# Performance work log

Measured on AMD Instinct MI355X. Metric: run time of the kernel, lower is better.

Reference implementation:

```python
import jax, jax.numpy as jnp
import numpy as np

N, E = 100000, 1600000
IN, HID, EMB = 128, 256, 64


def setup_inputs() -> dict:
    key = jax.random.key(0)
    ks = jax.random.split(key, 8)
    x = jax.random.normal(ks[0], (N, IN), dtype=jnp.float32)
    edge_index = jax.random.randint(ks[1], (2, E), 0, N, dtype=jnp.int64)
    def glorot(k, fan_in, fan_out):
        lim = np.sqrt(6.0 / (fan_in + fan_out)).astype(np.float32)
        return jax.random.uniform(k, (fan_in, fan_out), jnp.float32, -lim, lim)
    return {
        "x": x,
        "edge_index": edge_index,
        "W1": glorot(ks[2], IN, HID), "b1": jnp.zeros((HID,), jnp.float32),
        "W2": glorot(ks[3], HID, HID), "b2": jnp.zeros((HID,), jnp.float32),
        "W3": glorot(ks[4], HID, EMB), "b3": jnp.zeros((EMB,), jnp.float32),
    }


def reference(x, edge_index, W1, b1, W2, b2, W3, b3):
    n = x.shape[0]
    # add self loops (PyG GCNConv default, fill_value=1)
    loops = jnp.arange(n, dtype=edge_index.dtype)
    src = jnp.concatenate([edge_index[0], loops])
    dst = jnp.concatenate([edge_index[1], loops])
    # symmetric normalization D^-1/2 A_hat D^-1/2 (degree at target)
    deg = jax.ops.segment_sum(jnp.ones_like(src, dtype=x.dtype), dst, num_segments=n)
    dinv = jnp.where(deg > 0, deg ** -0.5, 0.0)
    norm = (dinv[src] * dinv[dst])[:, None]  # [E+N, 1]

    def conv(h, W, b):
        h = h @ W                               # [N, out]
        agg = jax.ops.segment_sum(h[src] * norm, dst, num_segments=n)
        return agg + b

    h = jax.nn.relu(conv(x, W1, b1))   # dropout: identity in eval mode
    h = jax.nn.relu(conv(h, W2, b2))
    h = conv(h, W3, b3)
    # L2-normalize rows (F.normalize, eps=1e-12)
    nrm = jnp.linalg.norm(h, axis=1, keepdims=True)
    return h / jnp.maximum(nrm, 1e-12)
```

## Files before the change

### kernel.cpp

```cpp
#include <hip/hip_runtime.h>
#include <cstddef>
#include <cstdint>

constexpr int IN_F  = 128;
constexpr int HID_F = 256;
constexpr int EMB_F = 64;

typedef float  f32x4  __attribute__((ext_vector_type(4)));
typedef short  bf16x8 __attribute__((ext_vector_type(8)));
typedef unsigned short ushort_t;
typedef ushort_t u16x4 __attribute__((ext_vector_type(4)));
typedef ushort_t u16x2 __attribute__((ext_vector_type(2)));

__device__ inline float bf2f(ushort_t u) {
  union { unsigned i; float f; } c; c.i = ((unsigned)u) << 16; return c.f;
}
__device__ inline ushort_t f2bf(float f) {
  union { float f; unsigned i; } c; c.f = f;
  unsigned r = c.i + 0x7FFFu + ((c.i >> 16) & 1u);
  return (ushort_t)(r >> 16);
}


__global__ void k_setup(const float* __restrict__ W1, const float* __restrict__ W2,
                        const float* __restrict__ W3,
                        ushort_t* __restrict__ W1t, ushort_t* __restrict__ W2t,
                        ushort_t* __restrict__ W3t) {
  constexpr int c1 = IN_F * HID_F;
  constexpr int c2 = c1 + HID_F * HID_F;
  constexpr int c3 = c2 + HID_F * EMB_F;
  int i = blockIdx.x * blockDim.x + threadIdx.x;
  if (i < c1) {
    int k = i / HID_F, nn = i - k * HID_F;
    W1t[(size_t)nn * IN_F + k] = f2bf(W1[i]);
  } else if (i < c2) {
    int j = i - c1;
    int k = j / HID_F, nn = j - k * HID_F;
    W2t[(size_t)nn * HID_F + k] = f2bf(W2[j]);
  } else if (i < c3) {
    int j = i - c2;
    int k = j / EMB_F, nn = j - k * EMB_F;
    W3t[(size_t)nn * HID_F + k] = f2bf(W3[j]);
  }
}


constexpr int NBKT = 512;
constexpr int CHUNK = 16384;

__global__ __launch_bounds__(512) void k_hist(const int* __restrict__ dst,
                                              int* __restrict__ ghist, int e) {
  __shared__ int cnt[NBKT];
  cnt[threadIdx.x] = 0;
  __syncthreads();
  int i0 = blockIdx.x * CHUNK;
  int i1 = min(e, i0 + CHUNK);
  for (int i = i0 + threadIdx.x; i < i1; i += 512)
    atomicAdd(&cnt[dst[i] >> 8], 1);
  __syncthreads();
  int c = cnt[threadIdx.x];
  if (c > 0) atomicAdd(&ghist[threadIdx.x], c);
}

__global__ __launch_bounds__(512) void k_bscan(const int* __restrict__ ghist,
                                               int* __restrict__ bstart,
                                               int* __restrict__ gcursor) {
  __shared__ int s[NBKT];
  int v = ghist[threadIdx.x];
  s[threadIdx.x] = v;
  __syncthreads();
#pragma unroll
  for (int off = 1; off < NBKT; off <<= 1) {
    int t = (threadIdx.x >= off) ? s[threadIdx.x - off] : 0;
    __syncthreads();
    s[threadIdx.x] += t;
    __syncthreads();
  }
  int ex = s[threadIdx.x] - v;
  bstart[threadIdx.x] = ex;
  gcursor[threadIdx.x] = ex;
}

__global__ __launch_bounds__(512) void k_passA(const int* __restrict__ src,
                                               const int* __restrict__ dst,
                                               int* __restrict__ gcursor,
                                               unsigned* __restrict__ staged, int e) {
  __shared__ int cnt[NBKT];
  __shared__ int base[NBKT];
  cnt[threadIdx.x] = 0;
  __syncthreads();
  int i0 = blockIdx.x * CHUNK;
  int i1 = min(e, i0 + CHUNK);
  for (int i = i0 + threadIdx.x; i < i1; i += 512)
    atomicAdd(&cnt[dst[i] >> 8], 1);
  __syncthreads();
  int c = cnt[threadIdx.x];
  base[threadIdx.x] = (c > 0) ? atomicAdd(&gcursor[threadIdx.x], c) : 0;
  cnt[threadIdx.x] = 0;
  __syncthreads();
  for (int i = i0 + threadIdx.x; i < i1; i += 512) {
    int d = dst[i];
    int b = d >> 8;
    int lp = atomicAdd(&cnt[b], 1);
    staged[base[b] + lp] = ((unsigned)(d & 255) << 17) | (unsigned)src[i];
  }
}

__global__ __launch_bounds__(256) void k_B1(const unsigned* __restrict__ staged,
                                            const int* __restrict__ bstart,
                                            const int* __restrict__ ghist,
                                            int* __restrict__ edgedeg,
                                            float* __restrict__ dinv, int n) {
  __shared__ int cnt[256];
  cnt[threadIdx.x] = 0;
  __syncthreads();
  int b = blockIdx.x;
  int beg = bstart[b], end = beg + ghist[b];
  for (int i = beg + threadIdx.x; i < end; i += 256)
    atomicAdd(&cnt[staged[i] >> 17], 1);
  __syncthreads();
  int node = (b << 8) + threadIdx.x;
  if (node < n) {
    int c = cnt[threadIdx.x];
    edgedeg[node] = c;
    dinv[node] = rsqrtf((float)(c + 1));
  }
}

__global__ __launch_bounds__(256) void k_B2(const unsigned* __restrict__ staged,
                                            const int* __restrict__ bstart,
                                            const int* __restrict__ ghist,
                                            const int* __restrict__ rowptr,
                                            int* __restrict__ csr, int n) {
  __shared__ int cur[256];
  cur[threadIdx.x] = 0;
  __syncthreads();
  int b = blockIdx.x;
  int beg = bstart[b], end = beg + ghist[b];
  int nb0 = b << 8;
  for (int i = beg + threadIdx.x; i < end; i += 256) {
    unsigned p = staged[i];
    int l = (int)(p >> 17);
    int s = (int)(p & 0x1FFFFu);
    int pos = rowptr[nb0 + l] + atomicAdd(&cur[l], 1);
    csr[pos] = s;
  }
}


__global__ void k_scan1(const int* __restrict__ edgedeg, int* __restrict__ rowptr,
                        int* __restrict__ bsum, int n) {
  __shared__ int s[256];
  int i = blockIdx.x * 256 + threadIdx.x;
  int v = (i < n) ? edgedeg[i] : 0;
  s[threadIdx.x] = v;
  __syncthreads();
#pragma unroll
  for (int off = 1; off < 256; off <<= 1) {
    int t = (threadIdx.x >= off) ? s[threadIdx.x - off] : 0;
    __syncthreads();
    s[threadIdx.x] += t;
    __syncthreads();
  }
  if (i < n) rowptr[i] = s[threadIdx.x] - v;
  if (threadIdx.x == 255) bsum[blockIdx.x] = s[255];
}

__global__ void k_scan2(int* __restrict__ bsum, int nb) {
  __shared__ int s[512];
  int v = (threadIdx.x < nb) ? bsum[threadIdx.x] : 0;
  s[threadIdx.x] = v;
  __syncthreads();
#pragma unroll
  for (int off = 1; off < 512; off <<= 1) {
    int t = (threadIdx.x >= off) ? s[threadIdx.x - off] : 0;
    __syncthreads();
    s[threadIdx.x] += t;
    __syncthreads();
  }
  if (threadIdx.x < nb) bsum[threadIdx.x] = s[threadIdx.x] - v;
}

__global__ void k_scan3(int* __restrict__ rowptr, const int* __restrict__ bsum,
                        int n, int e) {
  int i = blockIdx.x * blockDim.x + threadIdx.x;
  if (i < n) rowptr[i] += bsum[i >> 8];
  else if (i == n) rowptr[n] = e;
}


__global__ void k_xconv(const float* __restrict__ x, const float* __restrict__ dinv,
                        ushort_t* __restrict__ xb, int n4 ) {
  int i = blockIdx.x * blockDim.x + threadIdx.x;
  if (i >= n4) return;
  float s = dinv[i >> 5];
  float4 v = reinterpret_cast<const float4*>(x)[i];
  u16x4 o;
  o[0] = f2bf(v.x * s); o[1] = f2bf(v.y * s); o[2] = f2bf(v.z * s); o[3] = f2bf(v.w * s);
  reinterpret_cast<u16x4*>(xb)[i] = o;
}


__global__ __launch_bounds__(256) void k_gather1(
    const ushort_t* __restrict__ t, ushort_t* __restrict__ outp,
    const int* __restrict__ rowptr, const int* __restrict__ csr, int n) {
  int wid = (blockIdx.x * blockDim.x + threadIdx.x) >> 6;
  int lane = threadIdx.x & 63;
  if (wid >= n) return;
  float a0, a1;
  {
    u16x2 v = *reinterpret_cast<const u16x2*>(t + (size_t)wid * IN_F + lane * 2);
    a0 = bf2f(v[0]); a1 = bf2f(v[1]);
  }
  int beg = rowptr[wid], end = rowptr[wid + 1];
  int j = beg;
  for (; j + 3 < end; j += 4) {
    int s0 = csr[j], s1 = csr[j + 1], s2 = csr[j + 2], s3 = csr[j + 3];
    u16x2 v0 = *reinterpret_cast<const u16x2*>(t + (size_t)s0 * IN_F + lane * 2);
    u16x2 v1 = *reinterpret_cast<const u16x2*>(t + (size_t)s1 * IN_F + lane * 2);
    u16x2 v2 = *reinterpret_cast<const u16x2*>(t + (size_t)s2 * IN_F + lane * 2);
    u16x2 v3 = *reinterpret_cast<const u16x2*>(t + (size_t)s3 * IN_F + lane * 2);
    a0 += bf2f(v0[0]); a1 += bf2f(v0[1]);
    a0 += bf2f(v1[0]); a1 += bf2f(v1[1]);
    a0 += bf2f(v2[0]); a1 += bf2f(v2[1]);
    a0 += bf2f(v3[0]); a1 += bf2f(v3[1]);
  }
  for (; j < end; ++j) {
    int s0 = csr[j];
    u16x2 v0 = *reinterpret_cast<const u16x2*>(t + (size_t)s0 * IN_F + lane * 2);
    a0 += bf2f(v0[0]); a1 += bf2f(v0[1]);
  }
  u16x2 o; o[0] = f2bf(a0); o[1] = f2bf(a1);
  *reinterpret_cast<u16x2*>(outp + (size_t)wid * IN_F + lane * 2) = o;
}

__global__ __launch_bounds__(256) void k_gather2(
    const ushort_t* __restrict__ t, ushort_t* __restrict__ outp,
    const int* __restrict__ rowptr, const int* __restrict__ csr,
    const float* __restrict__ dinv, const float* __restrict__ bias, int n) {
  int wid = (blockIdx.x * blockDim.x + threadIdx.x) >> 6;
  int lane = threadIdx.x & 63;
  if (wid >= n) return;
  float acc[4];
  {
    u16x4 v = *reinterpret_cast<const u16x4*>(t + (size_t)wid * HID_F + lane * 4);
#pragma unroll
    for (int k = 0; k < 4; ++k) acc[k] = bf2f(v[k]);
  }
  int beg = rowptr[wid], end = rowptr[wid + 1];
  int j = beg;
  for (; j + 3 < end; j += 4) {
    int s0 = csr[j], s1 = csr[j + 1], s2 = csr[j + 2], s3 = csr[j + 3];
    u16x4 v0 = *reinterpret_cast<const u16x4*>(t + (size_t)s0 * HID_F + lane * 4);
    u16x4 v1 = *reinterpret_cast<const u16x4*>(t + (size_t)s1 * HID_F + lane * 4);
    u16x4 v2 = *reinterpret_cast<const u16x4*>(t + (size_t)s2 * HID_F + lane * 4);
    u16x4 v3 = *reinterpret_cast<const u16x4*>(t + (size_t)s3 * HID_F + lane * 4);
#pragma unroll
    for (int k = 0; k < 4; ++k) acc[k] += bf2f(v0[k]);
#pragma unroll
    for (int k = 0; k < 4; ++k) acc[k] += bf2f(v1[k]);
#pragma unroll
    for (int k = 0; k < 4; ++k) acc[k] += bf2f(v2[k]);
#pragma unroll
    for (int k = 0; k < 4; ++k) acc[k] += bf2f(v3[k]);
  }
  for (; j < end; ++j) {
    int s0 = csr[j];
    u16x4 v0 = *reinterpret_cast<const u16x4*>(t + (size_t)s0 * HID_F + lane * 4);
#pragma unroll
    for (int k = 0; k < 4; ++k) acc[k] += bf2f(v0[k]);
  }
  float s = dinv[wid];
  int c = lane * 4;
  u16x4 o;
#pragma unroll
  for (int k = 0; k < 4; ++k) o[k] = f2bf(fmaxf(fmaf(acc[k], s, bias[c + k]), 0.f));
  *reinterpret_cast<u16x4*>(outp + (size_t)wid * HID_F + lane * 4) = o;
}

__global__ __launch_bounds__(256) void k_gather3(
    const ushort_t* __restrict__ t, float* __restrict__ outp,
    const int* __restrict__ rowptr, const int* __restrict__ csr,
    const float* __restrict__ dinv, const float* __restrict__ b3, int n) {
  int wid = (blockIdx.x * blockDim.x + threadIdx.x) >> 6;
  int lane = threadIdx.x & 63;
  if (wid >= n) return;
  float a = bf2f(t[(size_t)wid * EMB_F + lane]);
  int beg = rowptr[wid], end = rowptr[wid + 1];
  int j = beg;
  for (; j + 3 < end; j += 4) {
    int s0 = csr[j], s1 = csr[j + 1], s2 = csr[j + 2], s3 = csr[j + 3];
    float v0 = bf2f(t[(size_t)s0 * EMB_F + lane]);
    float v1 = bf2f(t[(size_t)s1 * EMB_F + lane]);
    float v2 = bf2f(t[(size_t)s2 * EMB_F + lane]);
    float v3 = bf2f(t[(size_t)s3 * EMB_F + lane]);
    a += v0; a += v1; a += v2; a += v3;
  }
  for (; j < end; ++j) a += bf2f(t[(size_t)csr[j] * EMB_F + lane]);
  float v = fmaf(a, dinv[wid], b3[lane]);
  float ss = v * v;
#pragma unroll
  for (int off = 32; off > 0; off >>= 1) ss += __shfl_xor(ss, off);
  float nrm = sqrtf(ss);
  outp[(size_t)wid * EMB_F + lane] = v / fmaxf(nrm, 1e-12f);
}


template<int K, bool RELU>
__global__ __launch_bounds__(256) void k_mfma_gemm(
    const ushort_t* __restrict__ A, const ushort_t* __restrict__ Wt,
    ushort_t* __restrict__ C,
    const float* __restrict__ dinv, const float* __restrict__ bias,
    int M, int NT ) {
  int w = blockIdx.x * 4 + (threadIdx.x >> 6);
  int lane = threadIdx.x & 63;
  int mt = w / NT, nt = w - mt * NT;
  int mbase = mt * 64, nbase = nt * 64;
  if (mbase >= M) return;
  const int lrow = lane & 15;
  const int lk = (lane >> 4) * 8;
  const int N = NT * 64;

  int rows[4];
#pragma unroll
  for (int i = 0; i < 4; ++i) {
    int r = mbase + i * 16 + lrow;
    rows[i] = (r < M) ? r : (M - 1);
  }

  f32x4 acc[4][4] = {};

#pragma unroll 2
  for (int k0 = 0; k0 < K; k0 += 32) {
    bf16x8 a[4], b[4];
#pragma unroll
    for (int i = 0; i < 4; ++i)
      a[i] = *reinterpret_cast<const bf16x8*>(A + (size_t)rows[i] * K + k0 + lk);
#pragma unroll
    for (int n = 0; n < 4; ++n)
      b[n] = *reinterpret_cast<const bf16x8*>(Wt + (size_t)(nbase + n * 16 + lrow) * K + k0 + lk);
#pragma unroll
    for (int i = 0; i < 4; ++i)
#pragma unroll
      for (int n = 0; n < 4; ++n)
        acc[i][n] = __builtin_amdgcn_mfma_f32_16x16x32_bf16(a[i], b[n], acc[i][n], 0, 0, 0);
  }

#pragma unroll
  for (int i = 0; i < 4; ++i) {
    int growb = mbase + i * 16 + (lane >> 4) * 4;
#pragma unroll
    for (int r = 0; r < 4; ++r) {
      int grow = growb + r;
      if (grow >= M) continue;
      float s = dinv[grow];
#pragma unroll
      for (int n = 0; n < 4; ++n) {
        int gcol = nbase + n * 16 + (lane & 15);
        float v = acc[i][n][r] * s;
        if (RELU) v = fmaxf(v + bias[gcol], 0.f);
        C[(size_t)grow * N + gcol] = f2bf(v);
      }
    }
  }
}


extern "C" void kernel_launch(void* const* d_in, const int* in_sizes, int n_in,
                              void* d_out, int out_size, void* d_ws, size_t ws_size,
                              hipStream_t stream) {
  const float* x  = (const float*)d_in[0];
  const int*   ei = (const int*)d_in[1];
  const float* W1 = (const float*)d_in[2];
  const float* b1 = (const float*)d_in[3];
  const float* W2 = (const float*)d_in[4];
  const float* b2 = (const float*)d_in[5];
  const float* W3 = (const float*)d_in[6];
  const float* b3 = (const float*)d_in[7];
  const int N = in_sizes[0] / IN_F;
  const int E = in_sizes[1] / 2;
  const int* src = ei;
  const int* dst = ei + E;

  char* m = (char*)d_ws;
  auto alloc = [&](size_t bytes) { char* p = m; m += (bytes + 255) & ~(size_t)255; return p; };
  ushort_t* U1  = (ushort_t*)alloc((size_t)N * HID_F * 2);
  ushort_t* U2  = (ushort_t*)alloc((size_t)N * HID_F * 2);
  ushort_t* W1t = (ushort_t*)alloc((size_t)IN_F * HID_F * 2);
  ushort_t* W2t = (ushort_t*)alloc((size_t)HID_F * HID_F * 2);
  ushort_t* W3t = (ushort_t*)alloc((size_t)HID_F * EMB_F * 2);
  int*      edgedeg = (int*)alloc((size_t)N * 4);
  float*    dinv    = (float*)alloc((size_t)N * 4);
  int*      rowptr  = (int*)alloc((size_t)(N + 1) * 4);
  int*      bsum    = (int*)alloc(512 * 4);
  int*      ghist   = (int*)alloc(NBKT * 4);
  int*      bstart  = (int*)alloc(NBKT * 4);
  int*      gcursor = (int*)alloc(NBKT * 4);
  unsigned* staged  = (unsigned*)alloc((size_t)E * 4);
  int*      csr     = (int*)alloc((size_t)E * 4);
  float*    out     = (float*)d_out;

  const int nb = (N + 255) / 256;
  const int nbkt_used = (N + 255) / 256;
  const int echunks = (E + CHUNK - 1) / CHUNK;
  constexpr int SETUP_W = IN_F * HID_F + HID_F * HID_F + HID_F * EMB_F;

  k_setup<<<(SETUP_W + 255) / 256, 256, 0, stream>>>(W1, W2, W3, W1t, W2t, W3t);

  hipMemsetAsync(ghist, 0, NBKT * 4, stream);
  k_hist <<<echunks, 512, 0, stream>>>(dst, ghist, E);
  k_bscan<<<1, NBKT, 0, stream>>>(ghist, bstart, gcursor);
  k_passA<<<echunks, 512, 0, stream>>>(src, dst, gcursor, staged, E);
  k_B1   <<<nbkt_used, 256, 0, stream>>>(staged, bstart, ghist, edgedeg, dinv, N);

  k_scan1<<<nb, 256, 0, stream>>>(edgedeg, rowptr, bsum, N);
  k_scan2<<<1, 512, 0, stream>>>(bsum, nb);
  k_scan3<<<(N + 1 + 255) / 256, 256, 0, stream>>>(rowptr, bsum, N, E);

  ushort_t* xb = U2;
  k_xconv<<<((N * 32) + 255) / 256, 256, 0, stream>>>(x, dinv, xb, N * 32);

  k_B2<<<nbkt_used, 256, 0, stream>>>(staged, bstart, ghist, rowptr, csr, N);

  const int gblocks = (N + 3) / 4;
  const int MT = (N + 63) / 64;

  ushort_t* aggX = U1;
  k_gather1<<<gblocks, 256, 0, stream>>>(xb, aggX, rowptr, csr, N);
  ushort_t* h1 = U2;
  k_mfma_gemm<IN_F, true><<<(MT * (HID_F / 64) + 3) / 4, 256, 0, stream>>>(
      aggX, W1t, h1, dinv, b1, N, HID_F / 64);

  ushort_t* t2 = U1;
  k_mfma_gemm<HID_F, false><<<(MT * (HID_F / 64) + 3) / 4, 256, 0, stream>>>(
      h1, W2t, t2, dinv, nullptr, N, HID_F / 64);
  ushort_t* h2 = U2;
  k_gather2<<<gblocks, 256, 0, stream>>>(t2, h2, rowptr, csr, dinv, b2, N);

  ushort_t* t3 = U1;
  k_mfma_gemm<HID_F, false><<<(MT * (EMB_F / 64) + 3) / 4, 256, 0, stream>>>(
      h2, W3t, t3, dinv, nullptr, N, EMB_F / 64);
  k_gather3<<<gblocks, 256, 0, stream>>>(t3, out, rowptr, csr, dinv, b3, N);
}
```

Measured before the change: 473.0 us.

## Fuse preprocessing kernels and widen gather loads with split-wave edge parallelism

Folds the ghist memset into the weight-setup kernel and the per-block degree scan into the bucket-count kernel. It also merges the rowptr fixup with the x bf16 conversion, which removes several launches and the edgedeg buffer. The three gather kernels now have each half or quarter of a wave handle different neighbors using wider 8- or 16-byte vector loads, then combine partial sums with cross-lane shuffles. This aims to raise memory-level parallelism in the gathers, at the cost of extra shuffles and idle lanes when degree is low.

New measurement: 469.4 us. Within noise of the previous version (-0.8%).

```diff
diff --git a/kernel.cpp b/kernel.cpp
--- a/kernel.cpp
+++ b/kernel.cpp
@@ -9,8 +9,8 @@
 typedef float  f32x4  __attribute__((ext_vector_type(4)));
 typedef short  bf16x8 __attribute__((ext_vector_type(8)));
 typedef unsigned short ushort_t;
+typedef ushort_t u16x8 __attribute__((ext_vector_type(8)));
 typedef ushort_t u16x4 __attribute__((ext_vector_type(4)));
-typedef ushort_t u16x2 __attribute__((ext_vector_type(2)));
 
 __device__ inline float bf2f(ushort_t u) {
   union { unsigned i; float f; } c; c.i = ((unsigned)u) << 16; return c.f;
@@ -21,11 +21,14 @@
   return (ushort_t)(r >> 16);
 }
 
+constexpr int NBKT = 512;
+constexpr int CHUNK = 16384;
+
 
 __global__ void k_setup(const float* __restrict__ W1, const float* __restrict__ W2,
                         const float* __restrict__ W3,
                         ushort_t* __restrict__ W1t, ushort_t* __restrict__ W2t,
-                        ushort_t* __restrict__ W3t) {
+                        ushort_t* __restrict__ W3t, int* __restrict__ ghist) {
   constexpr int c1 = IN_F * HID_F;
   constexpr int c2 = c1 + HID_F * HID_F;
   constexpr int c3 = c2 + HID_F * EMB_F;
@@ -41,12 +44,11 @@
     int j = i - c2;
     int k = j / EMB_F, nn = j - k * EMB_F;
     W3t[(size_t)nn * HID_F + k] = f2bf(W3[j]);
-  }
-}
-
-
-constexpr int NBKT = 512;
-constexpr int CHUNK = 16384;
+  } else if (i - c3 < NBKT) {
+    ghist[i - c3] = 0;
+  }
+}
+
 
 __global__ __launch_bounds__(512) void k_hist(const int* __restrict__ dst,
                                               int* __restrict__ ghist, int e) {
@@ -106,12 +108,14 @@
   }
 }
 
-__global__ __launch_bounds__(256) void k_B1(const unsigned* __restrict__ staged,
-                                            const int* __restrict__ bstart,
-                                            const int* __restrict__ ghist,
-                                            int* __restrict__ edgedeg,
-                                            float* __restrict__ dinv, int n) {
+__global__ __launch_bounds__(256) void k_B1scan(const unsigned* __restrict__ staged,
+                                                const int* __restrict__ bstart,
+                                                const int* __restrict__ ghist,
+                                                float* __restrict__ dinv,
+                                                int* __restrict__ rowptr,
+                                                int* __restrict__ bsum, int n) {
   __shared__ int cnt[256];
+  __shared__ int s[256];
   cnt[threadIdx.x] = 0;
   __syncthreads();
   int b = blockIdx.x;
@@ -120,10 +124,51 @@
     atomicAdd(&cnt[staged[i] >> 17], 1);
   __syncthreads();
   int node = (b << 8) + threadIdx.x;
-  if (node < n) {
-    int c = cnt[threadIdx.x];
-    edgedeg[node] = c;
-    dinv[node] = rsqrtf((float)(c + 1));
+  int v = (node < n) ? cnt[threadIdx.x] : 0;
+  if (node < n) dinv[node] = rsqrtf((float)(v + 1));
+  s[threadIdx.x] = v;
+  __syncthreads();
+#pragma unroll
+  for (int off = 1; off < 256; off <<= 1) {
+    int t = (threadIdx.x >= off) ? s[threadIdx.x - off] : 0;
+    __syncthreads();
+    s[threadIdx.x] += t;
+    __syncthreads();
+  }
+  if (node < n) rowptr[node] = s[threadIdx.x] - v;
+  if (threadIdx.x == 255) bsum[b] = s[255];
+}
+
+__global__ void k_scan2(int* __restrict__ bsum, int nb) {
+  __shared__ int s[512];
+  int v = (threadIdx.x < nb) ? bsum[threadIdx.x] : 0;
+  s[threadIdx.x] = v;
+  __syncthreads();
+#pragma unroll
+  for (int off = 1; off < 512; off <<= 1) {
+    int t = (threadIdx.x >= off) ? s[threadIdx.x - off] : 0;
+    __syncthreads();
+    s[threadIdx.x] += t;
+    __syncthreads();
+  }
+  if (threadIdx.x < nb) bsum[threadIdx.x] = s[threadIdx.x] - v;
+}
+
+__global__ void k_scan3x(int* __restrict__ rowptr, const int* __restrict__ bsum,
+                         const float* __restrict__ x, const float* __restrict__ dinv,
+                         ushort_t* __restrict__ xb, int n, int e) {
+  int i = blockIdx.x * blockDim.x + threadIdx.x;
+  int n32 = n * 32;
+  if (i < n32) {
+    float s = dinv[i >> 5];
+    float4 v = reinterpret_cast<const float4*>(x)[i];
+    u16x4 o;
+    o[0] = f2bf(v.x * s); o[1] = f2bf(v.y * s); o[2] = f2bf(v.z * s); o[3] = f2bf(v.w * s);
+    reinterpret_cast<u16x4*>(xb)[i] = o;
+  } else {
+    int j = i - n32;
+    if (j < n) rowptr[j] += bsum[j >> 8];
+    else if (j == n) rowptr[n] = e;
   }
 }
 
@@ -148,90 +193,46 @@
 }
 
 
-__global__ void k_scan1(const int* __restrict__ edgedeg, int* __restrict__ rowptr,
-                        int* __restrict__ bsum, int n) {
-  __shared__ int s[256];
-  int i = blockIdx.x * 256 + threadIdx.x;
-  int v = (i < n) ? edgedeg[i] : 0;
-  s[threadIdx.x] = v;
-  __syncthreads();
-#pragma unroll
-  for (int off = 1; off < 256; off <<= 1) {
-    int t = (threadIdx.x >= off) ? s[threadIdx.x - off] : 0;
-    __syncthreads();
-    s[threadIdx.x] += t;
-    __syncthreads();
-  }
-  if (i < n) rowptr[i] = s[threadIdx.x] - v;
-  if (threadIdx.x == 255) bsum[blockIdx.x] = s[255];
-}
-
-__global__ void k_scan2(int* __restrict__ bsum, int nb) {
-  __shared__ int s[512];
-  int v = (threadIdx.x < nb) ? bsum[threadIdx.x] : 0;
-  s[threadIdx.x] = v;
-  __syncthreads();
-#pragma unroll
-  for (int off = 1; off < 512; off <<= 1) {
-    int t = (threadIdx.x >= off) ? s[threadIdx.x - off] : 0;
-    __syncthreads();
-    s[threadIdx.x] += t;
-    __syncthreads();
-  }
-  if (threadIdx.x < nb) bsum[threadIdx.x] = s[threadIdx.x] - v;
-}
-
-__global__ void k_scan3(int* __restrict__ rowptr, const int* __restrict__ bsum,
-                        int n, int e) {
-  int i = blockIdx.x * blockDim.x + threadIdx.x;
-  if (i < n) rowptr[i] += bsum[i >> 8];
-  else if (i == n) rowptr[n] = e;
-}
-
-
-__global__ void k_xconv(const float* __restrict__ x, const float* __restrict__ dinv,
-                        ushort_t* __restrict__ xb, int n4 ) {
-  int i = blockIdx.x * blockDim.x + threadIdx.x;
-  if (i >= n4) return;
-  float s = dinv[i >> 5];
-  float4 v = reinterpret_cast<const float4*>(x)[i];
-  u16x4 o;
-  o[0] = f2bf(v.x * s); o[1] = f2bf(v.y * s); o[2] = f2bf(v.z * s); o[3] = f2bf(v.w * s);
-  reinterpret_cast<u16x4*>(xb)[i] = o;
-}
-
-
 __global__ __launch_bounds__(256) void k_gather1(
     const ushort_t* __restrict__ t, ushort_t* __restrict__ outp,
     const int* __restrict__ rowptr, const int* __restrict__ csr, int n) {
   int wid = (blockIdx.x * blockDim.x + threadIdx.x) >> 6;
   int lane = threadIdx.x & 63;
   if (wid >= n) return;
-  float a0, a1;
-  {
-    u16x2 v = *reinterpret_cast<const u16x2*>(t + (size_t)wid * IN_F + lane * 2);
-    a0 = bf2f(v[0]); a1 = bf2f(v[1]);
-  }
+  const int half = lane >> 5, sub = lane & 31;
+  const int coff = sub * 4;
   int beg = rowptr[wid], end = rowptr[wid + 1];
-  int j = beg;
-  for (; j + 3 < end; j += 4) {
-    int s0 = csr[j], s1 = csr[j + 1], s2 = csr[j + 2], s3 = csr[j + 3];
-    u16x2 v0 = *reinterpret_cast<const u16x2*>(t + (size_t)s0 * IN_F + lane * 2);
-    u16x2 v1 = *reinterpret_cast<const u16x2*>(t + (size_t)s1 * IN_F + lane * 2);
-    u16x2 v2 = *reinterpret_cast<const u16x2*>(t + (size_t)s2 * IN_F + lane * 2);
-    u16x2 v3 = *reinterpret_cast<const u16x2*>(t + (size_t)s3 * IN_F + lane * 2);
-    a0 += bf2f(v0[0]); a1 += bf2f(v0[1]);
-    a0 += bf2f(v1[0]); a1 += bf2f(v1[1]);
-    a0 += bf2f(v2[0]); a1 += bf2f(v2[1]);
-    a0 += bf2f(v3[0]); a1 += bf2f(v3[1]);
-  }
-  for (; j < end; ++j) {
-    int s0 = csr[j];
-    u16x2 v0 = *reinterpret_cast<const u16x2*>(t + (size_t)s0 * IN_F + lane * 2);
-    a0 += bf2f(v0[0]); a1 += bf2f(v0[1]);
-  }
-  u16x2 o; o[0] = f2bf(a0); o[1] = f2bf(a1);
-  *reinterpret_cast<u16x2*>(outp + (size_t)wid * IN_F + lane * 2) = o;
+  int nitems = end - beg + 1;
+  float acc[4] = {};
+  int i = 0;
+  for (; i + 3 < nitems; i += 4) {
+    int i0 = i + half, i1 = i + 2 + half;
+    int r0 = (i0 == 0) ? wid : csr[beg + i0 - 1];
+    int r1 = csr[beg + i1 - 1];
+    u16x4 v0 = *reinterpret_cast<const u16x4*>(t + (size_t)r0 * IN_F + coff);
+    u16x4 v1 = *reinterpret_cast<const u16x4*>(t + (size_t)r1 * IN_F + coff);
+#pragma unroll
+    for (int k = 0; k < 4; ++k) acc[k] += bf2f(v0[k]);
+#pragma unroll
+    for (int k = 0; k < 4; ++k) acc[k] += bf2f(v1[k]);
+  }
+  for (; i < nitems; i += 2) {
+    int i0 = i + half;
+    if (i0 < nitems) {
+      int r0 = (i0 == 0) ? wid : csr[beg + i0 - 1];
+      u16x4 v0 = *reinterpret_cast<const u16x4*>(t + (size_t)r0 * IN_F + coff);
+#pragma unroll
+      for (int k = 0; k < 4; ++k) acc[k] += bf2f(v0[k]);
+    }
+  }
+#pragma unroll
+  for (int k = 0; k < 4; ++k) acc[k] += __shfl_xor(acc[k], 32);
+  if (half == 0) {
+    u16x4 o;
+#pragma unroll
+    for (int k = 0; k < 4; ++k) o[k] = f2bf(acc[k]);
+    *reinterpret_cast<u16x4*>(outp + (size_t)wid * IN_F + coff) = o;
+  }
 }
 
 __global__ __launch_bounds__(256) void k_gather2(
@@ -241,41 +242,41 @@
   int wid = (blockIdx.x * blockDim.x + threadIdx.x) >> 6;
   int lane = threadIdx.x & 63;
   if (wid >= n) return;
-  float acc[4];
-  {
-    u16x4 v = *reinterpret_cast<const u16x4*>(t + (size_t)wid * HID_F + lane * 4);
-#pragma unroll
-    for (int k = 0; k < 4; ++k) acc[k] = bf2f(v[k]);
-  }
+  const int half = lane >> 5, sub = lane & 31;
+  const int coff = sub * 8;
   int beg = rowptr[wid], end = rowptr[wid + 1];
-  int j = beg;
-  for (; j + 3 < end; j += 4) {
-    int s0 = csr[j], s1 = csr[j + 1], s2 = csr[j + 2], s3 = csr[j + 3];
-    u16x4 v0 = *reinterpret_cast<const u16x4*>(t + (size_t)s0 * HID_F + lane * 4);
-    u16x4 v1 = *reinterpret_cast<const u16x4*>(t + (size_t)s1 * HID_F + lane * 4);
-    u16x4 v2 = *reinterpret_cast<const u16x4*>(t + (size_t)s2 * HID_F + lane * 4);
-    u16x4 v3 = *reinterpret_cast<const u16x4*>(t + (size_t)s3 * HID_F + lane * 4);
-#pragma unroll
-    for (int k = 0; k < 4; ++k) acc[k] += bf2f(v0[k]);
-#pragma unroll
-    for (int k = 0; k < 4; ++k) acc[k] += bf2f(v1[k]);
-#pragma unroll
-    for (int k = 0; k < 4; ++k) acc[k] += bf2f(v2[k]);
-#pragma unroll
-    for (int k = 0; k < 4; ++k) acc[k] += bf2f(v3[k]);
-  }
-  for (; j < end; ++j) {
-    int s0 = csr[j];
-    u16x4 v0 = *reinterpret_cast<const u16x4*>(t + (size_t)s0 * HID_F + lane * 4);
-#pragma unroll
-    for (int k = 0; k < 4; ++k) acc[k] += bf2f(v0[k]);
-  }
-  float s = dinv[wid];
-  int c = lane * 4;
-  u16x4 o;
-#pragma unroll
-  for (int k = 0; k < 4; ++k) o[k] = f2bf(fmaxf(fmaf(acc[k], s, bias[c + k]), 0.f));
-  *reinterpret_cast<u16x4*>(outp + (size_t)wid * HID_F + lane * 4) = o;
+  int nitems = end - beg + 1;
+  float acc[8] = {};
+  int i = 0;
+  for (; i + 3 < nitems; i += 4) {
+    int i0 = i + half, i1 = i + 2 + half;
+    int r0 = (i0 == 0) ? wid : csr[beg + i0 - 1];
+    int r1 = csr[beg + i1 - 1];
+    u16x8 v0 = *reinterpret_cast<const u16x8*>(t + (size_t)r0 * HID_F + coff);
+    u16x8 v1 = *reinterpret_cast<const u16x8*>(t + (size_t)r1 * HID_F + coff);
+#pragma unroll
+    for (int k = 0; k < 8; ++k) acc[k] += bf2f(v0[k]);
+#pragma unroll
+    for (int k = 0; k < 8; ++k) acc[k] += bf2f(v1[k]);
+  }
+  for (; i < nitems; i += 2) {
+    int i0 = i + half;
+    if (i0 < nitems) {
+      int r0 = (i0 == 0) ? wid : csr[beg + i0 - 1];
+      u16x8 v0 = *reinterpret_cast<const u16x8*>(t + (size_t)r0 * HID_F + coff);
+#pragma unroll
+      for (int k = 0; k < 8; ++k) acc[k] += bf2f(v0[k]);
+    }
+  }
+#pragma unroll
+  for (int k = 0; k < 8; ++k) acc[k] += __shfl_xor(acc[k], 32);
+  if (half == 0) {
+    float s = dinv[wid];
+    u16x8 o;
+#pragma unroll
+    for (int k = 0; k < 8; ++k) o[k] = f2bf(fmaxf(fmaf(acc[k], s, bias[coff + k]), 0.f));
+    *reinterpret_cast<u16x8*>(outp + (size_t)wid * HID_F + coff) = o;
+  }
 }
 
 __global__ __launch_bounds__(256) void k_gather3(
@@ -285,24 +286,38 @@
   int wid = (blockIdx.x * blockDim.x + threadIdx.x) >> 6;
   int lane = threadIdx.x & 63;
   if (wid >= n) return;
-  float a = bf2f(t[(size_t)wid * EMB_F + lane]);
+  const int q = lane >> 4, sub = lane & 15;
+  const int coff = sub * 4;
   int beg = rowptr[wid], end = rowptr[wid + 1];
-  int j = beg;
-  for (; j + 3 < end; j += 4) {
-    int s0 = csr[j], s1 = csr[j + 1], s2 = csr[j + 2], s3 = csr[j + 3];
-    float v0 = bf2f(t[(size_t)s0 * EMB_F + lane]);
-    float v1 = bf2f(t[(size_t)s1 * EMB_F + lane]);
-    float v2 = bf2f(t[(size_t)s2 * EMB_F + lane]);
-    float v3 = bf2f(t[(size_t)s3 * EMB_F + lane]);
-    a += v0; a += v1; a += v2; a += v3;
-  }
-  for (; j < end; ++j) a += bf2f(t[(size_t)csr[j] * EMB_F + lane]);
-  float v = fmaf(a, dinv[wid], b3[lane]);
-  float ss = v * v;
-#pragma unroll
-  for (int off = 32; off > 0; off >>= 1) ss += __shfl_xor(ss, off);
-  float nrm = sqrtf(ss);
-  outp[(size_t)wid * EMB_F + lane] = v / fmaxf(nrm, 1e-12f);
+  int nitems = end - beg + 1;
+  float acc[4] = {};
+  for (int i = 0; i < nitems; i += 4) {
+    int i0 = i + q;
+    if (i0 < nitems) {
+      int r0 = (i0 == 0) ? wid : csr[beg + i0 - 1];
+      u16x4 v0 = *reinterpret_cast<const u16x4*>(t + (size_t)r0 * EMB_F + coff);
+#pragma unroll
+      for (int k = 0; k < 4; ++k) acc[k] += bf2f(v0[k]);
+    }
+  }
+#pragma unroll
+  for (int k = 0; k < 4; ++k) acc[k] += __shfl_xor(acc[k], 16);
+#pragma unroll
+  for (int k = 0; k < 4; ++k) acc[k] += __shfl_xor(acc[k], 32);
+  float s = dinv[wid];
+  float v[4], ss = 0.f;
+#pragma unroll
+  for (int k = 0; k < 4; ++k) {
+    v[k] = fmaf(acc[k], s, b3[coff + k]);
+    ss = fmaf(v[k], v[k], ss);
+  }
+#pragma unroll
+  for (int off = 8; off > 0; off >>= 1) ss += __shfl_xor(ss, off);
+  float inv = 1.0f / fmaxf(sqrtf(ss), 1e-12f);
+  if (lane < 16) {
+    float4 o = make_float4(v[0] * inv, v[1] * inv, v[2] * inv, v[3] * inv);
+    *reinterpret_cast<float4*>(outp + (size_t)wid * EMB_F + coff) = o;
+  }
 }
 
 
@@ -389,7 +404,6 @@
   ushort_t* W1t = (ushort_t*)alloc((size_t)IN_F * HID_F * 2);
   ushort_t* W2t = (ushort_t*)alloc((size_t)HID_F * HID_F * 2);
   ushort_t* W3t = (ushort_t*)alloc((size_t)HID_F * EMB_F * 2);
-  int*      edgedeg = (int*)alloc((size_t)N * 4);
   float*    dinv    = (float*)alloc((size_t)N * 4);
   int*      rowptr  = (int*)alloc((size_t)(N + 1) * 4);
   int*      bsum    = (int*)alloc(512 * 4);
@@ -401,26 +415,21 @@
   float*    out     = (float*)d_out;
 
   const int nb = (N + 255) / 256;
-  const int nbkt_used = (N + 255) / 256;
   const int echunks = (E + CHUNK - 1) / CHUNK;
-  constexpr int SETUP_W = IN_F * HID_F + HID_F * HID_F + HID_F * EMB_F;
-
-  k_setup<<<(SETUP_W + 255) / 256, 256, 0, stream>>>(W1, W2, W3, W1t, W2t, W3t);
-
-  hipMemsetAsync(ghist, 0, NBKT * 4, stream);
-  k_hist <<<echunks, 512, 0, stream>>>(dst, ghist, E);
-  k_bscan<<<1, NBKT, 0, stream>>>(ghist, bstart, gcursor);
-  k_passA<<<echunks, 512, 0, stream>>>(src, dst, gcursor, staged, E);
-  k_B1   <<<nbkt_used, 256, 0, stream>>>(staged, bstart, ghist, edgedeg, dinv, N);
-
-  k_scan1<<<nb, 256, 0, stream>>>(edgedeg, rowptr, bsum, N);
-  k_scan2<<<1, 512, 0, stream>>>(bsum, nb);
-  k_scan3<<<(N + 1 + 255) / 256, 256, 0, stream>>>(rowptr, bsum, N, E);
+  constexpr int SETUP_W = IN_F * HID_F + HID_F * HID_F + HID_F * EMB_F + NBKT;
+
+  k_setup<<<(SETUP_W + 255) / 256, 256, 0, stream>>>(W1, W2, W3, W1t, W2t, W3t, ghist);
+
+  k_hist  <<<echunks, 512, 0, stream>>>(dst, ghist, E);
+  k_bscan <<<1, NBKT, 0, stream>>>(ghist, bstart, gcursor);
+  k_passA <<<echunks, 512, 0, stream>>>(src, dst, gcursor, staged, E);
+  k_B1scan<<<nb, 256, 0, stream>>>(staged, bstart, ghist, dinv, rowptr, bsum, N);
+  k_scan2 <<<1, 512, 0, stream>>>(bsum, nb);
 
   ushort_t* xb = U2;
-  k_xconv<<<((N * 32) + 255) / 256, 256, 0, stream>>>(x, dinv, xb, N * 32);
-
-  k_B2<<<nbkt_used, 256, 0, stream>>>(staged, bstart, ghist, rowptr, csr, N);
+  k_scan3x<<<((N * 32) + N + 1 + 255) / 256, 256, 0, stream>>>(rowptr, bsum, x, dinv, xb, N, E);
+
+  k_B2<<<nb, 256, 0, stream>>>(staged, bstart, ghist, rowptr, csr, N);
 
   const int gblocks = (N + 3) / 4;
   const int MT = (N + 63) / 64;
```
